# Performance work log

Hardware: AMD Instinct MI355X
Metric: run time of the kernel (lower is better)

## Reference

```python
import jax, jax.numpy as jnp
import numpy as np

DIM = 64
NUM_FEAT = 14
NUM_OUT = 105
N_NODES = 8192
N_EDGES = 16384
N_GRAPHS = 256
N_STEMS = 2048
N_JBONDS = 1024


def lrelu(v):
    return jax.nn.leaky_relu(v, 0.01)


def setup_inputs() -> dict:
    key = jax.random.key(0)
    ks = jax.random.split(key, 40)
    def rn(k, shape, s=0.1):
        return jax.random.normal(k, shape, dtype=jnp.float32) * s
    inp = {}
    inp['x'] = jax.random.normal(ks[0], (N_NODES, NUM_FEAT), dtype=jnp.float32)
    inp['edge_attr'] = jax.random.uniform(ks[1], (N_EDGES, 4), dtype=jnp.float32)
    inp['edge_index'] = jax.random.randint(ks[2], (2, N_EDGES), 0, N_NODES)
    inp['batch'] = jnp.sort(jax.random.randint(ks[3], (N_NODES,), 0, N_GRAPHS))
    inp['stem_atmidx'] = jax.random.randint(ks[4], (N_STEMS,), 0, N_NODES)
    inp['jbond_atmidx'] = jax.random.randint(ks[5], (N_JBONDS, 2), 0, N_NODES)
    # lin0
    inp['lin0_w'] = rn(ks[6], (NUM_FEAT, DIM)); inp['lin0_b'] = rn(ks[7], (DIM,))
    # NNConv edge net: Linear(4,dim) -> LeakyReLU -> Linear(dim, dim*dim)
    inp['net_w1'] = rn(ks[8], (4, DIM)); inp['net_b1'] = rn(ks[9], (DIM,))
    inp['net_w2'] = rn(ks[10], (DIM, DIM * DIM), 0.02); inp['net_b2'] = rn(ks[11], (DIM * DIM,), 0.02)
    # NNConv root weight + bias
    inp['conv_root'] = rn(ks[12], (DIM, DIM)); inp['conv_bias'] = rn(ks[13], (DIM,))
    # GRU (torch gate order r,z,n); stored [in, 3*dim]
    inp['gru_w_ih'] = rn(ks[14], (DIM, 3 * DIM)); inp['gru_w_hh'] = rn(ks[15], (DIM, 3 * DIM))
    inp['gru_b_ih'] = rn(ks[16], (3 * DIM,)); inp['gru_b_hh'] = rn(ks[17], (3 * DIM,))
    # node2stem MLP
    inp['n2s_w1'] = rn(ks[18], (DIM, DIM)); inp['n2s_b1'] = rn(ks[19], (DIM,))
    inp['n2s_w2'] = rn(ks[20], (DIM, NUM_OUT)); inp['n2s_b2'] = rn(ks[21], (NUM_OUT,))
    # node2jbond MLP
    inp['n2j_w1'] = rn(ks[22], (DIM, DIM)); inp['n2j_b1'] = rn(ks[23], (DIM,))
    inp['n2j_w2'] = rn(ks[24], (DIM, 1)); inp['n2j_b2'] = rn(ks[25], (1,))
    # Set2Set LSTM(2*dim -> dim), torch gate order i,f,g,o; stored [in, 4*dim]
    inp['s2s_w_ih'] = rn(ks[26], (2 * DIM, 4 * DIM)); inp['s2s_w_hh'] = rn(ks[27], (DIM, 4 * DIM))
    inp['s2s_b_ih'] = rn(ks[28], (4 * DIM,)); inp['s2s_b_hh'] = rn(ks[29], (4 * DIM,))
    # lin_out
    inp['lin_out_w'] = rn(ks[30], (2 * DIM, 2)); inp['lin_out_b'] = rn(ks[31], (2,))
    return inp


def reference(x, edge_attr, lin0_w, lin0_b, net_w1, net_b1, net_w2, net_b2,
              conv_root, conv_bias, gru_w_ih, gru_w_hh, gru_b_ih, gru_b_hh,
              n2s_w1, n2s_b1, n2s_w2, n2s_b2, n2j_w1, n2j_b1, n2j_w2, n2j_b2,
              s2s_w_ih, s2s_w_hh, s2s_b_ih, s2s_b_hh, lin_out_w, lin_out_b,
              edge_index, batch, stem_atmidx, jbond_atmidx):
    N = x.shape[0]
    src, dst = edge_index[0], edge_index[1]
    out = lrelu(x @ lin0_w + lin0_b)          # [N, dim]
    h = out
    # edge-conditioned weights (edge_attr is constant across the 6 iterations)
    ew = (lrelu(edge_attr @ net_w1 + net_b1) @ net_w2 + net_b2).reshape(-1, DIM, DIM)  # [E,dim,dim]
    deg = jnp.maximum(jax.ops.segment_sum(jnp.ones_like(dst, dtype=x.dtype), dst, num_segments=N), 1.0)[:, None]
    for _ in range(6):
        msg = jnp.einsum('ei,eio->eo', out[src], ew)                        # per-edge matmul
        agg = jax.ops.segment_sum(msg, dst, num_segments=N) / deg          # scatter-mean
        m = lrelu(agg + out @ conv_root + conv_bias)
        # GRU update (torch gate order r,z,n)
        gi = m @ gru_w_ih + gru_b_ih
        gh = h @ gru_w_hh + gru_b_hh
        ir, iz, inn = jnp.split(gi, 3, axis=-1)
        hr, hz, hn = jnp.split(gh, 3, axis=-1)
        r = jax.nn.sigmoid(ir + hr)
        z = jax.nn.sigmoid(iz + hz)
        n = jnp.tanh(inn + r * hn)
        h = (1.0 - z) * n + z * h
        out = h
    # per-stem block logits
    stem_preds = lrelu(out[stem_atmidx] @ n2s_w1 + n2s_b1) @ n2s_w2 + n2s_b2  # [S, num_out]
    # jbond: gather both endpoints, predict scalar, mean over the pair
    jb = out[jbond_atmidx.reshape(-1)]
    jpred = lrelu(jb @ n2j_w1 + n2j_b1) @ n2j_w2 + n2j_b2                     # [2J,1]
    jbond_preds = jpred.reshape(jbond_atmidx.shape).mean(axis=1)              # [J]
    # Set2Set, processing_steps=1
    B = N_GRAPHS
    hS = jnp.zeros((B, DIM), x.dtype)
    cS = jnp.zeros((B, DIM), x.dtype)
    q_star = jnp.zeros((B, 2 * DIM), x.dtype)
    gates = q_star @ s2s_w_ih + s2s_b_ih + hS @ s2s_w_hh + s2s_b_hh
    gi_, gf_, gg_, go_ = jnp.split(gates, 4, axis=-1)
    cS = jax.nn.sigmoid(gf_) * cS + jax.nn.sigmoid(gi_) * jnp.tanh(gg_)
    hS = jax.nn.sigmoid(go_) * jnp.tanh(cS)
    q = hS                                                                    # [B, dim]
    e = jnp.sum(out * q[batch], axis=-1)                                      # [N]
    emax = jax.ops.segment_max(e, batch, num_segments=B)
    a_un = jnp.exp(e - emax[batch])
    a = a_un / jax.ops.segment_sum(a_un, batch, num_segments=B)[batch]
    r_pool = jax.ops.segment_sum(a[:, None] * out, batch, num_segments=B)     # [B, dim]
    q_star = jnp.concatenate([q, r_pool], axis=1)                             # [B, 2*dim]
    scalar_outs = q_star @ lin_out_w + lin_out_b                              # [B, 2]
    return (scalar_outs, stem_preds, jbond_preds)
```

## Files before the change

### kernel.cpp

```cpp
#include <hip/hip_runtime.h>

#define DIM 64
#define NF 14
#define NOUT 105
#define NN 8192
#define NE 16384
#define NB 256
#define NS 2048
#define NJ 1024
#define KTOT 4160
#define KSPLIT 8

#define C_X      0
#define C_EA     114688
#define C_L0W    180224
#define C_L0B    181120
#define C_NW1    181184
#define C_NB1    181440
#define C_NW2    181504
#define C_NB2    443648
#define C_CRT    447744
#define C_CB     451840
#define C_GWIH   451904
#define C_GWHH   464192
#define C_GBIH   476480
#define C_GBHH   476672
#define C_SW1    476864
#define C_SB1    480960
#define C_SW2    481024
#define C_SB2    487744
#define C_JW1    487856
#define C_JB1    491952
#define C_JW2    492016
#define C_JB2    492080
#define C_S2IH   492088
#define C_S2HH   492344
#define C_LOW    492600
#define C_LOB    492856
#define C_TOT    492864

typedef float f32x4 __attribute__((ext_vector_type(4)));
typedef short bf16x8 __attribute__((ext_vector_type(8)));

__device__ __forceinline__ float bf2f(unsigned short u){
  union { unsigned int i; float f; } v; v.i = ((unsigned int)u) << 16; return v.f;
}
__device__ __forceinline__ unsigned short f2bf(float f){
  union { float f; unsigned int i; } v; v.f = f;
  unsigned int x = v.i;
  return (unsigned short)((x + 0x7FFFu + ((x >> 16) & 1u)) >> 16);
}
__device__ __forceinline__ float sigm(float x){ return 1.f / (1.f + __expf(-x)); }
__device__ __forceinline__ float tanh_f(float x){
  x = fminf(10.f, fmaxf(-10.f, x));
  float e = __expf(2.f * x);
  return (e - 1.f) / (e + 1.f);
}
__device__ __forceinline__ float lrelu(float x){ return x > 0.f ? x : 0.01f * x; }

__device__ __forceinline__ float wred_sum(float v){
  #pragma unroll
  for (int off = 32; off > 0; off >>= 1) v += __shfl_xor(v, off, 64);
  return v;
}
__device__ __forceinline__ float wred_max(float v){
  #pragma unroll
  for (int off = 32; off > 0; off >>= 1) v = fmaxf(v, __shfl_xor(v, off, 64));
  return v;
}


__global__ void k_detect(const unsigned short* __restrict__ ea, int* __restrict__ flag){
  __shared__ int cnt;
  if (threadIdx.x == 0) cnt = 0;
  __syncthreads();
  int c = 0;
  for (int i = threadIdx.x; i < 8192; i += 256) c += (ea[2*i] >> 15) & 1;
  atomicAdd(&cnt, c);
  __syncthreads();
  if (threadIdx.x == 0) *flag = (cnt > 100) ? 1 : 0;
}

struct CvtArgs {
  const void* src[26];
  int n[26];
  int off[26];
};

__global__ void k_cvt(CvtArgs a, const int* __restrict__ flag, unsigned short* __restrict__ dst){
  bool f32 = (*flag != 0);
  int gid = blockIdx.x * blockDim.x + threadIdx.x, gs = gridDim.x * blockDim.x;
  #pragma unroll 1
  for (int j = 0; j < 26; ++j){
    const void* s = a.src[j];
    int n = a.n[j], o = a.off[j];
    for (int i = gid; i < n; i += gs)
      dst[o + i] = f32 ? f2bf(((const float*)s)[i]) : ((const unsigned short*)s)[i];
  }
}

#define SETUP_BLOCKS 7249

__global__ __launch_bounds__(256) void k_setup(const unsigned short* __restrict__ cvt,
                       const int* __restrict__ ei, int big,
                       float* __restrict__ deg,
                       float* __restrict__ actF, unsigned short* __restrict__ actB,
                       unsigned short* __restrict__ z,
                       unsigned short* __restrict__ w2t, unsigned short* __restrict__ w2rt,
                       unsigned short* __restrict__ crt, unsigned short* __restrict__ btg,
                       float* __restrict__ cbg, float* __restrict__ qv){
  int bid = blockIdx.x, tid = threadIdx.x;
  if (bid < 2048){
    const unsigned short* x = cvt + C_X;
    const unsigned short* w = cvt + C_L0W;
    const unsigned short* b = cvt + C_L0B;
    int idx = bid * 256 + tid;
    int n = idx >> 6, d = idx & 63;
    float acc = bf2f(b[d]);
    #pragma unroll
    for (int f = 0; f < NF; ++f) acc += bf2f(x[n*NF + f]) * bf2f(w[f*DIM + d]);
    float v = lrelu(acc);
    actF[idx] = v; actB[idx] = f2bf(v);
  } else if (bid < 6144){
    const unsigned short* ea = cvt + C_EA;
    const unsigned short* w  = cvt + C_NW1;
    const unsigned short* b  = cvt + C_NB1;
    int idx = (bid - 2048) * 256 + tid;
    int e = idx >> 6, d = idx & 63;
    float acc = bf2f(b[d]);
    #pragma unroll
    for (int f = 0; f < 4; ++f) acc += bf2f(ea[e*4 + f]) * bf2f(w[f*DIM + d]);
    z[idx] = f2bf(lrelu(acc));
  } else if (bid < 7184){
    int idx = (bid - 6144) * 256 + tid;
    const unsigned short* w2 = cvt + C_NW2;
    if (big){
      if (idx < 4096*64){
        int n = idx >> 6, k = idx & 63;
        int c = ((n & 63) << 6) | (n >> 6);
        w2t[idx] = w2[k*4096 + c];
      }
    } else {
      if (idx < 64*KTOT){
        const unsigned short* b2 = cvt + C_NB2;
        int o = idx / KTOT, k = idx - o * KTOT;
        w2rt[idx] = (k < 4096) ? w2[(k >> 6) * 4096 + (k & 63) * 64 + o]
                               : b2[(k - 4096) * 64 + o];
      }
    }
  } else if (bid < 7248){
    int e = (bid - 7184) * 256 + tid;
    if (e < NE) atomicAdd(&deg[ei[NE + e]], 1.0f);
  } else {
    const unsigned short* cr  = cvt + C_CRT;
    const unsigned short* wih = cvt + C_GWIH;
    const unsigned short* whh = cvt + C_GWHH;
    const unsigned short* bih = cvt + C_GBIH;
    const unsigned short* bhh = cvt + C_GBHH;
    const unsigned short* s2sbih = cvt + C_S2IH;
    const unsigned short* s2sbhh = cvt + C_S2HH;
    for (int t = tid; t < 4096; t += 256){ int n = t & 63, k = t >> 6; crt[n*64 + k] = cr[k*64 + n]; }
    for (int t = tid; t < 32768; t += 256){
      int nidx = t >> 7, kidx = t & 127;
      int g = nidx >> 6, d = nidx & 63, ki = kidx & 63;
      unsigned short v = 0;
      if (kidx < 64){
        if (g == 0) v = wih[ki*192 + d];
        else if (g == 1) v = wih[ki*192 + 64 + d];
        else if (g == 2) v = wih[ki*192 + 128 + d];
      } else {
        if (g == 0) v = whh[ki*192 + d];
        else if (g == 1) v = whh[ki*192 + 64 + d];
        else if (g == 3) v = whh[ki*192 + 128 + d];
      }
      btg[nidx*128 + kidx] = v;
    }
    if (tid < 256){
      int g = tid >> 6, d = tid & 63;
      float v;
      if (g == 0) v = bf2f(bih[d]) + bf2f(bhh[d]);
      else if (g == 1) v = bf2f(bih[64 + d]) + bf2f(bhh[64 + d]);
      else if (g == 2) v = bf2f(bih[128 + d]);
      else v = bf2f(bhh[128 + d]);
      cbg[tid] = v;
    }
    if (tid < 64){
      float gi = bf2f(s2sbih[tid])       + bf2f(s2sbhh[tid]);
      float gg = bf2f(s2sbih[128 + tid]) + bf2f(s2sbhh[128 + tid]);
      float go = bf2f(s2sbih[192 + tid]) + bf2f(s2sbhh[192 + tid]);
      float c = sigm(gi) * tanh_f(gg);
      qv[tid] = sigm(go) * tanh_f(c);
    }
  }
}


__global__ __launch_bounds__(256) void k_ew(const unsigned short* __restrict__ z,
                                            const unsigned short* __restrict__ w2t,
                                            const unsigned short* __restrict__ cvt,
                                            unsigned short* __restrict__ ew){
  const unsigned short* b2 = cvt + C_NB2;
  int w = threadIdx.x >> 6, lane = threadIdx.x & 63;
  int lm = lane & 15, q8 = (lane >> 4) * 8, rq = (lane >> 4) * 4;
  int e0 = blockIdx.x * 64;
  int n0 = blockIdx.y * 256 + w * 64;
  f32x4 acc[4][4];
  #pragma unroll
  for (int mt = 0; mt < 4; ++mt)
    #pragma unroll
    for (int nt = 0; nt < 4; ++nt) acc[mt][nt] = (f32x4){0.f, 0.f, 0.f, 0.f};
  #pragma unroll
  for (int kk = 0; kk < 2; ++kk){
    bf16x8 af[4], bfr[4];
    #pragma unroll
    for (int mt = 0; mt < 4; ++mt)
      af[mt] = *(const bf16x8*)&z[(size_t)(e0 + mt*16 + lm)*64 + kk*32 + q8];
    #pragma unroll
    for (int nt = 0; nt < 4; ++nt)
      bfr[nt] = *(const bf16x8*)&w2t[(size_t)(n0 + nt*16 + lm)*64 + kk*32 + q8];
    #pragma unroll
    for (int mt = 0; mt < 4; ++mt)
      #pragma unroll
      for (int nt = 0; nt < 4; ++nt)
        acc[mt][nt] = __builtin_amdgcn_mfma_f32_16x16x32_bf16(af[mt], bfr[nt], acc[mt][nt], 0, 0, 0);
  }
  float bb[4]; int cols[4];
  #pragma unroll
  for (int nt = 0; nt < 4; ++nt){
    int dp = n0 + nt*16 + lm;
    cols[nt] = dp;
    bb[nt] = bf2f(b2[((dp & 63) << 6) | (dp >> 6)]);
  }
  #pragma unroll
  for (int mt = 0; mt < 4; ++mt)
    #pragma unroll
    for (int r = 0; r < 4; ++r){
      size_t rowb = (size_t)(e0 + mt*16 + rq + r) * 4096;
      #pragma unroll
      for (int nt = 0; nt < 4; ++nt)
        ew[rowb + cols[nt]] = f2bf(acc[mt][nt][r] + bb[nt]);
    }
}

__global__ __launch_bounds__(256) void k_msg(const float* __restrict__ actF,
                                             const unsigned short* __restrict__ ew,
                                             const int* __restrict__ ei,
                                             float* __restrict__ agg){
  int w = threadIdx.x >> 6, lane = threadIdx.x & 63;
  int e = blockIdx.x * 4 + w;
  int src = ei[e], dst = ei[NE + e];
  int g = lane >> 3;
  int s8 = (lane & 7) * 8;
  f32x4 a0 = *(const f32x4*)&actF[(size_t)src*64 + s8];
  f32x4 a1 = *(const f32x4*)&actF[(size_t)src*64 + s8 + 4];
  const unsigned short* ep = ew + (size_t)e * 4096;
  float po[8];
  #pragma unroll
  for (int j = 0; j < 8; ++j){
    bf16x8 v = *(const bf16x8*)&ep[(size_t)(j*8 + g)*64 + s8];
    const unsigned int* dw = (const unsigned int*)&v;
    float acc = 0.f;
    #pragma unroll
    for (int h = 0; h < 4; ++h){
      float flo = __uint_as_float(dw[h] << 16);
      float fhi = __uint_as_float(dw[h] & 0xFFFF0000u);
      float alo = (h < 2) ? a0[2*h]     : a1[2*h - 4];
      float ahi = (h < 2) ? a0[2*h + 1] : a1[2*h - 3];
      acc += flo * alo + fhi * ahi;
    }
    po[j] = acc;
  }
  #pragma unroll
  for (int j = 0; j < 8; ++j){
    po[j] += __shfl_xor(po[j], 1, 64);
    po[j] += __shfl_xor(po[j], 2, 64);
    po[j] += __shfl_xor(po[j], 4, 64);
  }
  if ((lane & 7) == 0){
    #pragma unroll
    for (int j = 0; j < 8; ++j)
      atomicAdd(&agg[(size_t)dst*64 + j*8 + g], po[j]);
  }
}


__global__ __launch_bounds__(256) void k_msgf(const unsigned short* __restrict__ actB,
                                              const unsigned short* __restrict__ z,
                                              const unsigned short* __restrict__ w2rt,
                                              const int* __restrict__ ei,
                                              float* __restrict__ agg){
  __shared__ __align__(16) unsigned short sz[256 * 8];
  int w = threadIdx.x >> 6, lane = threadIdx.x & 63;
  int lm = lane & 15, q8 = (lane >> 4) * 8, rq = (lane >> 4) * 4;
  int e0 = blockIdx.x * 256;
  int s  = blockIdx.y;
  {
    int t = threadIdx.x;
    *(uint4*)&sz[t * 8] = *(const uint4*)&z[(size_t)(e0 + t) * 64 + s * 8];
  }
  __syncthreads();

  uint4 apack[4][2];
  #pragma unroll
  for (int mt = 0; mt < 4; ++mt){
    int src = ei[e0 + w*64 + mt*16 + lm];
    apack[mt][0] = *(const uint4*)&actB[(size_t)src * 64 + q8];
    apack[mt][1] = *(const uint4*)&actB[(size_t)src * 64 + 32 + q8];
  }

  f32x4 acc[4][4];
  #pragma unroll
  for (int mt = 0; mt < 4; ++mt)
    #pragma unroll
    for (int nt = 0; nt < 4; ++nt) acc[mt][nt] = (f32x4){0.f, 0.f, 0.f, 0.f};

  int kk0 = s * 16;
  int nk = (s == KSPLIT - 1) ? 18 : 16;
  for (int c = 0; c < nk; ++c){
    int kk = kk0 + c;
    bf16x8 bfr[4];
    #pragma unroll
    for (int nt = 0; nt < 4; ++nt)
      bfr[nt] = *(const bf16x8*)&w2rt[(size_t)(nt*16 + lm) * KTOT + kk*32 + q8];
    #pragma unroll
    for (int mt = 0; mt < 4; ++mt){
      float zf = 1.0f;
      if (kk < 128){
        int erow = w*64 + mt*16 + lm;
        zf = bf2f(sz[erow * 8 + ((kk >> 1) & 7)]);
      }
      uint4 ap = apack[mt][kk & 1];
      bf16x8 af;
      #pragma unroll
      for (int h = 0; h < 4; ++h){
        unsigned int dw = ((const unsigned int*)&ap)[h];
        float flo = __uint_as_float(dw << 16) * zf;
        float fhi = __uint_as_float(dw & 0xFFFF0000u) * zf;
        unsigned int pk = ((unsigned int)f2bf(flo)) | (((unsigned int)f2bf(fhi)) << 16);
        ((unsigned int*)&af)[h] = pk;
      }
      #pragma unroll
      for (int nt = 0; nt < 4; ++nt)
        acc[mt][nt] = __builtin_amdgcn_mfma_f32_16x16x32_bf16(af, bfr[nt], acc[mt][nt], 0, 0, 0);
    }
  }

  #pragma unroll
  for (int mt = 0; mt < 4; ++mt){
    int dstv[4];
    #pragma unroll
    for (int r = 0; r < 4; ++r) dstv[r] = ei[NE + e0 + w*64 + mt*16 + rq + r];
    #pragma unroll
    for (int nt = 0; nt < 4; ++nt)
      #pragma unroll
      for (int r = 0; r < 4; ++r)
        atomicAdd(&agg[(size_t)dstv[r] * 64 + nt*16 + lm], acc[mt][nt][r]);
  }
}


__global__ __launch_bounds__(256) void k_gru(const unsigned short* __restrict__ actB_in,
                                             const float* __restrict__ actF_in,
                                             float* __restrict__ agg, const float* __restrict__ deg,
                                             const unsigned short* __restrict__ crt,
                                             const unsigned short* __restrict__ cvt,
                                             const unsigned short* __restrict__ btg,
                                             const float* __restrict__ cbg,
                                             float* __restrict__ actF_out, unsigned short* __restrict__ actB_out){
  const unsigned short* cbias = cvt + C_CB;
  __shared__ __align__(16) unsigned short s_frag[2*4*16*8];
  int w = threadIdx.x >> 6, lane = threadIdx.x & 63;
  int lm = lane & 15, q = lane >> 4;
  int q8 = q*8, rq = q*4;
  int r0 = blockIdx.x * 16;
  f32x4 am = (f32x4){0.f, 0.f, 0.f, 0.f};
  #pragma unroll
  for (int kk = 0; kk < 2; ++kk){
    bf16x8 a = *(const bf16x8*)&actB_in[(size_t)(r0 + lm)*64 + kk*32 + q8];
    bf16x8 b = *(const bf16x8*)&crt[(size_t)(w*16 + lm)*64 + kk*32 + q8];
    am = __builtin_amdgcn_mfma_f32_16x16x32_bf16(a, b, am, 0, 0, 0);
  }
  {
    int col = w*16 + lm;
    float cb = bf2f(cbias[col]);
    int kk2 = w >> 1, q2 = (w & 1)*2 + (lm >> 3), j = lm & 7;
    #pragma unroll
    for (int r = 0; r < 4; ++r){
      int row = r0 + rq + r;
      float dg = fmaxf(deg[row], 1.f);
      float v = am[r] + agg[(size_t)row*64 + col] / dg + cb;
      agg[(size_t)row*64 + col] = 0.f;
      s_frag[((kk2*4 + q2)*16 + (rq + r))*8 + j] = f2bf(lrelu(v));
    }
  }
  __syncthreads();
  f32x4 g[4];
  #pragma unroll
  for (int t = 0; t < 4; ++t) g[t] = (f32x4){0.f, 0.f, 0.f, 0.f};
  #pragma unroll
  for (int kk = 0; kk < 4; ++kk){
    bf16x8 a;
    if (kk < 2) a = *(const bf16x8*)&s_frag[(kk*4 + q)*128 + lm*8];
    else        a = *(const bf16x8*)&actB_in[(size_t)(r0 + lm)*64 + (kk - 2)*32 + q8];
    #pragma unroll
    for (int t = 0; t < 4; ++t){
      bf16x8 b = *(const bf16x8*)&btg[(size_t)(t*64 + w*16 + lm)*128 + kk*32 + q8];
      g[t] = __builtin_amdgcn_mfma_f32_16x16x32_bf16(a, b, g[t], 0, 0, 0);
    }
  }
  {
    int d = w*16 + lm;
    float cb_r = cbg[d], cb_z = cbg[64 + d], cb_n = cbg[128 + d], cb_h = cbg[192 + d];
    #pragma unroll
    for (int r = 0; r < 4; ++r){
      int row = r0 + rq + r;
      float rr = sigm(g[0][r] + cb_r);
      float zz = sigm(g[1][r] + cb_z);
      float nn = tanh_f(g[2][r] + cb_n + rr * (g[3][r] + cb_h));
      float ho = actF_in[(size_t)row*64 + d];
      float hn2 = (1.f - zz) * nn + zz * ho;
      actF_out[(size_t)row*64 + d] = hn2;
      actB_out[(size_t)row*64 + d] = f2bf(hn2);
    }
  }
}


__device__ __forceinline__ int lower_bound_batch(const int* b, int val){
  int lo = 0, hi = NN;
  while (lo < hi){ int mid = (lo + hi) >> 1; if (b[mid] < val) lo = mid + 1; else hi = mid; }
  return lo;
}

__device__ __forceinline__ void store_out(void* outp, const int* flag, size_t idx, float v){
  if (*flag) ((float*)outp)[idx] = v;
  else       ((unsigned short*)outp)[idx] = f2bf(v);
}

__global__ __launch_bounds__(256) void k_heads(const float* __restrict__ act,
                                               const int* __restrict__ batch,
                                               const float* __restrict__ qv,
                                               const int* __restrict__ sidx,
                                               const int* __restrict__ jidx,
                                               const unsigned short* __restrict__ cvt,
                                               const int* __restrict__ flag,
                                               void* __restrict__ outp){
  int bid = blockIdx.x;
  int w = threadIdx.x >> 6, lane = threadIdx.x & 63;
  if (bid < 512){
    const unsigned short* w1 = cvt + C_SW1;
    const unsigned short* b1 = cvt + C_SB1;
    const unsigned short* w2 = cvt + C_SW2;
    const unsigned short* b2 = cvt + C_SB2;
    __shared__ float sa[4][64], st[4][64];
    int s = bid * 4 + w;
    int a = sidx[s];
    sa[w][lane] = act[(size_t)a*64 + lane];
    __syncthreads();
    float t = bf2f(b1[lane]);
    #pragma unroll 8
    for (int i = 0; i < 64; ++i) t += sa[w][i] * bf2f(w1[i*64 + lane]);
    st[w][lane] = lrelu(t);
    __syncthreads();
    size_t base = 512 + (size_t)s * NOUT;
    float v = bf2f(b2[lane]);
    #pragma unroll 8
    for (int d = 0; d < 64; ++d) v += st[w][d] * bf2f(w2[d*NOUT + lane]);
    store_out(outp, flag, base + lane, v);
    int o2 = 64 + lane;
    if (o2 < NOUT){
      float v2 = bf2f(b2[o2]);
      #pragma unroll 8
      for (int d = 0; d < 64; ++d) v2 += st[w][d] * bf2f(w2[d*NOUT + o2]);
      store_out(outp, flag, base + o2, v2);
    }
  } else if (bid < 768){
    const unsigned short* w1 = cvt + C_JW1;
    const unsigned short* b1 = cvt + C_JB1;
    const unsigned short* w2 = cvt + C_JW2;
    const unsigned short* b2 = cvt + C_JB2;
    __shared__ float a0[4][64], a1[4][64];
    int j = (bid - 512) * 4 + w;
    int i0 = jidx[j*2], i1 = jidx[j*2 + 1];
    a0[w][lane] = act[(size_t)i0*64 + lane];
    a1[w][lane] = act[(size_t)i1*64 + lane];
    __syncthreads();
    float t0 = bf2f(b1[lane]), t1 = t0;
    #pragma unroll 8
    for (int i = 0; i < 64; ++i){
      float wv = bf2f(w1[i*64 + lane]);
      t0 += a0[w][i] * wv;
      t1 += a1[w][i] * wv;
    }
    t0 = lrelu(t0); t1 = lrelu(t1);
    float p = (t0 + t1) * bf2f(w2[lane]);
    p = wred_sum(p);
    if (lane == 0) store_out(outp, flag, 512 + (size_t)NS*NOUT + j, 0.5f * p + bf2f(b2[0]));
  } else {
    const unsigned short* lw = cvt + C_LOW;
    const unsigned short* lb = cvt + C_LOB;
    __shared__ float se[4][512];
    int b = (bid - 768) * 4 + w;
    int lo = lower_bound_batch(batch, b);
    int hi = lower_bound_batch(batch, b + 1);
    int cnt = hi - lo; if (cnt > 512) cnt = 512;
    float qvl = qv[lane];
    for (int ii = 0; ii < cnt; ++ii){
      float p = act[(size_t)(lo + ii)*64 + lane] * qvl;
      p = wred_sum(p);
      if (lane == 0) se[w][ii] = p;
    }
    __syncthreads();
    float em = -3.4e38f;
    for (int ii = lane; ii < cnt; ii += 64) em = fmaxf(em, se[w][ii]);
    em = wred_max(em);
    float sm = 0.f;
    for (int ii = lane; ii < cnt; ii += 64) sm += __expf(se[w][ii] - em);
    float denom = wred_sum(sm);
    float rp = 0.f;
    for (int ii = 0; ii < cnt; ++ii) rp += __expf(se[w][ii] - em) * act[(size_t)(lo + ii)*64 + lane];
    if (cnt > 0 && denom > 0.f) rp /= denom;
    float s0 = qvl*bf2f(lw[lane*2])     + rp*bf2f(lw[(64 + lane)*2]);
    float s1 = qvl*bf2f(lw[lane*2 + 1]) + rp*bf2f(lw[(64 + lane)*2 + 1]);
    s0 = wred_sum(s0); s1 = wred_sum(s1);
    if (lane == 0){
      store_out(outp, flag, b*2,     s0 + bf2f(lb[0]));
      store_out(outp, flag, b*2 + 1, s1 + bf2f(lb[1]));
    }
  }
}


extern "C" void kernel_launch(void* const* d_in, const int* in_sizes, int n_in,
                              void* d_out, int out_size, void* d_ws, size_t ws_size,
                              hipStream_t stream){
  (void)in_sizes; (void)n_in; (void)out_size;
  const int* edge_index = (const int*)d_in[2];
  const int* batch      = (const int*)d_in[3];
  const int* stem_idx   = (const int*)d_in[4];
  const int* jbond_idx  = (const int*)d_in[5];

  char* ws = (char*)d_ws;
  size_t off = 0;
  auto alloc = [&](size_t bytes) -> void* {
    void* p = ws + off; off += (bytes + 255) & ~(size_t)255; return p;
  };
  unsigned short* cvt  = (unsigned short*)alloc((size_t)C_TOT * 2);
  unsigned short* w2t  = (unsigned short*)alloc((size_t)4096 * 64 * 2);
  unsigned short* w2rt = (unsigned short*)alloc((size_t)64 * KTOT * 2);
  unsigned short* z_bf = (unsigned short*)alloc((size_t)NE * 64 * 2);
  float* actF0 = (float*)alloc((size_t)NN * 64 * 4);
  float* actF1 = (float*)alloc((size_t)NN * 64 * 4);
  unsigned short* actB0 = (unsigned short*)alloc((size_t)NN * 64 * 2);
  unsigned short* actB1 = (unsigned short*)alloc((size_t)NN * 64 * 2);
  float* deg  = (float*)alloc(NN * 4);
  float* agg  = (float*)alloc((size_t)NN * 64 * 4);
  unsigned short* crt = (unsigned short*)alloc(64 * 64 * 2);
  unsigned short* btg = (unsigned short*)alloc(256 * 128 * 2);
  float* cbg  = (float*)alloc(256 * 4);
  float* qv   = (float*)alloc(64 * 4);
  int* flag   = (int*)alloc(256);
  size_t ew_bytes = (size_t)NE * 4096 * 2;
  bool big = (off + ew_bytes) <= ws_size;
  unsigned short* ew = big ? (unsigned short*)alloc(ew_bytes) : nullptr;

  hipMemsetAsync(deg, 0, ((size_t)NN * 4) + ((size_t)NN * 64 * 4) + 256, stream);

  k_detect<<<1, 256, 0, stream>>>((const unsigned short*)d_in[1], flag);

  CvtArgs ca;
  const int srcIdx[26] = {0,1,6,7,8,9,10,11,12,13,14,15,16,17,18,19,20,21,22,23,24,25,28,29,30,31};
  const int ns[26]  = {114688,65536,896,64,256,64,262144,4096,4096,64,12288,12288,192,192,
                       4096,64,6720,105,4096,64,64,1,256,256,256,2};
  const int ofs[26] = {C_X,C_EA,C_L0W,C_L0B,C_NW1,C_NB1,C_NW2,C_NB2,C_CRT,C_CB,C_GWIH,C_GWHH,
                       C_GBIH,C_GBHH,C_SW1,C_SB1,C_SW2,C_SB2,C_JW1,C_JB1,C_JW2,C_JB2,
                       C_S2IH,C_S2HH,C_LOW,C_LOB};
  for (int j = 0; j < 26; ++j){ ca.src[j] = d_in[srcIdx[j]]; ca.n[j] = ns[j]; ca.off[j] = ofs[j]; }
  k_cvt<<<512, 256, 0, stream>>>(ca, flag, cvt);

  k_setup<<<SETUP_BLOCKS, 256, 0, stream>>>(cvt, edge_index, big ? 1 : 0, deg,
                                            actF0, actB0, z_bf, w2t, w2rt,
                                            crt, btg, cbg, qv);

  if (big)
    k_ew<<<dim3(NE/64, 16), 256, 0, stream>>>(z_bf, w2t, cvt, ew);

  for (int t = 0; t < 6; ++t){
    const float* aF_in  = (t & 1) ? actF1 : actF0;
    float* aF_out       = (t & 1) ? actF0 : actF1;
    const unsigned short* aB_in = (t & 1) ? actB1 : actB0;
    unsigned short* aB_out      = (t & 1) ? actB0 : actB1;
    if (big)
      k_msg<<<NE/4, 256, 0, stream>>>(aF_in, ew, edge_index, agg);
    else
      k_msgf<<<dim3(NE/256, KSPLIT), 256, 0, stream>>>(aB_in, z_bf, w2rt, edge_index, agg);
    k_gru<<<NN/16, 256, 0, stream>>>(aB_in, aF_in, agg, deg, crt, cvt, btg, cbg,
                                     aF_out, aB_out);
  }
  k_heads<<<832, 256, 0, stream>>>(actF0, batch, qv, stem_idx, jbond_idx, cvt, flag, d_out);
}
```

Before: 444.5 us.

## Replace atomic scatter aggregation with CSR-sorted messages and gather-reduce in GRU

Adds a single-block kernel that builds a CSR ordering of edges by destination and permutes z rows into sorted order, so the per-edge weight matrices are produced in destination order. The message kernel now writes per-edge messages without atomics, and the GRU kernel sums each node's contiguous messages, taking degree from the row pointers. This removes float atomic contention and the agg memset and deg pass. In exchange it adds a serial single-block CSR build and an extra message buffer round trip each step, and the k_msg inner loop now reads rows with a 128-byte lane stride.

```diff
diff --git a/kernel.cpp b/kernel.cpp
--- a/kernel.cpp
+++ b/kernel.cpp
@@ -99,11 +99,50 @@
   }
 }
 
-#define SETUP_BLOCKS 7249
+
+__global__ __launch_bounds__(1024) void k_csr(const int* __restrict__ ei,
+                                              int* __restrict__ rowptr, int* __restrict__ pos,
+                                              int* __restrict__ srcS, int* __restrict__ dstS){
+  __shared__ int cnt[NN];
+  __shared__ int part[1024];
+  int t = threadIdx.x;
+  for (int i = t; i < NN; i += 1024) cnt[i] = 0;
+  __syncthreads();
+  for (int e = t; e < NE; e += 1024) atomicAdd(&cnt[ei[NE + e]], 1);
+  __syncthreads();
+  int base = t * 8;
+  int loc[8];
+  int s = 0;
+  #pragma unroll
+  for (int k = 0; k < 8; ++k){ loc[k] = cnt[base + k]; s += loc[k]; }
+  part[t] = s;
+  __syncthreads();
+  for (int off = 1; off < 1024; off <<= 1){
+    int v = (t >= off) ? part[t - off] : 0;
+    __syncthreads();
+    part[t] += v;
+    __syncthreads();
+  }
+  int run = part[t] - s;
+  #pragma unroll
+  for (int k = 0; k < 8; ++k){ cnt[base + k] = run; run += loc[k]; }
+  __syncthreads();
+  for (int i = t; i < NN; i += 1024) rowptr[i] = cnt[i];
+  if (t == 0) rowptr[NN] = NE;
+  __syncthreads();
+  for (int e = t; e < NE; e += 1024){
+    int d = ei[NE + e];
+    int p = atomicAdd(&cnt[d], 1);
+    pos[e] = p;
+    srcS[p] = ei[e];
+    dstS[p] = d;
+  }
+}
+
+#define SETUP_BLOCKS 7185
 
 __global__ __launch_bounds__(256) void k_setup(const unsigned short* __restrict__ cvt,
-                       const int* __restrict__ ei, int big,
-                       float* __restrict__ deg,
+                       const int* __restrict__ pos, int big,
                        float* __restrict__ actF, unsigned short* __restrict__ actB,
                        unsigned short* __restrict__ z,
                        unsigned short* __restrict__ w2t, unsigned short* __restrict__ w2rt,
@@ -130,7 +169,7 @@
     float acc = bf2f(b[d]);
     #pragma unroll
     for (int f = 0; f < 4; ++f) acc += bf2f(ea[e*4 + f]) * bf2f(w[f*DIM + d]);
-    z[idx] = f2bf(lrelu(acc));
+    z[(size_t)pos[e]*64 + d] = f2bf(lrelu(acc));
   } else if (bid < 7184){
     int idx = (bid - 6144) * 256 + tid;
     const unsigned short* w2 = cvt + C_NW2;
@@ -148,9 +187,6 @@
                                : b2[(k - 4096) * 64 + o];
       }
     }
-  } else if (bid < 7248){
-    int e = (bid - 7184) * 256 + tid;
-    if (e < NE) atomicAdd(&deg[ei[NE + e]], 1.0f);
   } else {
     const unsigned short* cr  = cvt + C_CRT;
     const unsigned short* wih = cvt + C_GWIH;
@@ -244,50 +280,42 @@
 
 __global__ __launch_bounds__(256) void k_msg(const float* __restrict__ actF,
                                              const unsigned short* __restrict__ ew,
-                                             const int* __restrict__ ei,
-                                             float* __restrict__ agg){
+                                             const int* __restrict__ srcS,
+                                             float* __restrict__ msg){
+  __shared__ __align__(16) float sact[4][64];
   int w = threadIdx.x >> 6, lane = threadIdx.x & 63;
-  int e = blockIdx.x * 4 + w;
-  int src = ei[e], dst = ei[NE + e];
-  int g = lane >> 3;
-  int s8 = (lane & 7) * 8;
-  f32x4 a0 = *(const f32x4*)&actF[(size_t)src*64 + s8];
-  f32x4 a1 = *(const f32x4*)&actF[(size_t)src*64 + s8 + 4];
-  const unsigned short* ep = ew + (size_t)e * 4096;
-  float po[8];
+  int bid = blockIdx.x;
+  int swz = (bid & 7) * (NE/4/8) + (bid >> 3);
+  int slot = swz * 4 + w;
+  int src = srcS[slot];
+  sact[w][lane] = actF[(size_t)src*64 + lane];
+  __syncthreads();
+  const unsigned short* ep = ew + (size_t)slot * 4096;
+  float acc = 0.f;
   #pragma unroll
   for (int j = 0; j < 8; ++j){
-    bf16x8 v = *(const bf16x8*)&ep[(size_t)(j*8 + g)*64 + s8];
+    bf16x8 v = *(const bf16x8*)&ep[(size_t)lane*64 + j*8];
+    f32x4 alo = *(const f32x4*)&sact[w][j*8];
+    f32x4 ahi = *(const f32x4*)&sact[w][j*8 + 4];
     const unsigned int* dw = (const unsigned int*)&v;
-    float acc = 0.f;
-    #pragma unroll
-    for (int h = 0; h < 4; ++h){
-      float flo = __uint_as_float(dw[h] << 16);
-      float fhi = __uint_as_float(dw[h] & 0xFFFF0000u);
-      float alo = (h < 2) ? a0[2*h]     : a1[2*h - 4];
-      float ahi = (h < 2) ? a0[2*h + 1] : a1[2*h - 3];
-      acc += flo * alo + fhi * ahi;
-    }
-    po[j] = acc;
-  }
-  #pragma unroll
-  for (int j = 0; j < 8; ++j){
-    po[j] += __shfl_xor(po[j], 1, 64);
-    po[j] += __shfl_xor(po[j], 2, 64);
-    po[j] += __shfl_xor(po[j], 4, 64);
-  }
-  if ((lane & 7) == 0){
-    #pragma unroll
-    for (int j = 0; j < 8; ++j)
-      atomicAdd(&agg[(size_t)dst*64 + j*8 + g], po[j]);
-  }
+    acc += __uint_as_float(dw[0] << 16)          * alo[0];
+    acc += __uint_as_float(dw[0] & 0xFFFF0000u)  * alo[1];
+    acc += __uint_as_float(dw[1] << 16)          * alo[2];
+    acc += __uint_as_float(dw[1] & 0xFFFF0000u)  * alo[3];
+    acc += __uint_as_float(dw[2] << 16)          * ahi[0];
+    acc += __uint_as_float(dw[2] & 0xFFFF0000u)  * ahi[1];
+    acc += __uint_as_float(dw[3] << 16)          * ahi[2];
+    acc += __uint_as_float(dw[3] & 0xFFFF0000u)  * ahi[3];
+  }
+  msg[(size_t)slot*64 + lane] = acc;
 }
 
 
 __global__ __launch_bounds__(256) void k_msgf(const unsigned short* __restrict__ actB,
                                               const unsigned short* __restrict__ z,
                                               const unsigned short* __restrict__ w2rt,
-                                              const int* __restrict__ ei,
+                                              const int* __restrict__ srcS,
+                                              const int* __restrict__ dstS,
                                               float* __restrict__ agg){
   __shared__ __align__(16) unsigned short sz[256 * 8];
   int w = threadIdx.x >> 6, lane = threadIdx.x & 63;
@@ -303,7 +331,7 @@
   uint4 apack[4][2];
   #pragma unroll
   for (int mt = 0; mt < 4; ++mt){
-    int src = ei[e0 + w*64 + mt*16 + lm];
+    int src = srcS[e0 + w*64 + mt*16 + lm];
     apack[mt][0] = *(const uint4*)&actB[(size_t)src * 64 + q8];
     apack[mt][1] = *(const uint4*)&actB[(size_t)src * 64 + 32 + q8];
   }
@@ -349,7 +377,7 @@
   for (int mt = 0; mt < 4; ++mt){
     int dstv[4];
     #pragma unroll
-    for (int r = 0; r < 4; ++r) dstv[r] = ei[NE + e0 + w*64 + mt*16 + rq + r];
+    for (int r = 0; r < 4; ++r) dstv[r] = dstS[e0 + w*64 + mt*16 + rq + r];
     #pragma unroll
     for (int nt = 0; nt < 4; ++nt)
       #pragma unroll
@@ -361,7 +389,9 @@
 
 __global__ __launch_bounds__(256) void k_gru(const unsigned short* __restrict__ actB_in,
                                              const float* __restrict__ actF_in,
-                                             float* __restrict__ agg, const float* __restrict__ deg,
+                                             const float* __restrict__ msg,
+                                             const int* __restrict__ rowptr,
+                                             float* __restrict__ agg, int bigf,
                                              const unsigned short* __restrict__ crt,
                                              const unsigned short* __restrict__ cvt,
                                              const unsigned short* __restrict__ btg,
@@ -369,10 +399,30 @@
                                              float* __restrict__ actF_out, unsigned short* __restrict__ actB_out){
   const unsigned short* cbias = cvt + C_CB;
   __shared__ __align__(16) unsigned short s_frag[2*4*16*8];
+  __shared__ float aggT[16][65];
+  __shared__ int rp[17];
   int w = threadIdx.x >> 6, lane = threadIdx.x & 63;
   int lm = lane & 15, q = lane >> 4;
   int q8 = q*8, rq = q*4;
   int r0 = blockIdx.x * 16;
+  if (threadIdx.x < 17) rp[threadIdx.x] = rowptr[r0 + threadIdx.x];
+  __syncthreads();
+  if (bigf){
+    #pragma unroll
+    for (int k = 0; k < 4; ++k){
+      int ln = w*4 + k;
+      float acc = 0.f;
+      for (int s = rp[ln]; s < rp[ln+1]; ++s) acc += msg[(size_t)s*64 + lane];
+      aggT[ln][lane] = acc;
+    }
+  } else {
+    for (int idx = threadIdx.x; idx < 1024; idx += 256){
+      int ln = idx >> 6, c = idx & 63;
+      aggT[ln][c] = agg[(size_t)(r0+ln)*64 + c];
+      agg[(size_t)(r0+ln)*64 + c] = 0.f;
+    }
+  }
+  __syncthreads();
   f32x4 am = (f32x4){0.f, 0.f, 0.f, 0.f};
   #pragma unroll
   for (int kk = 0; kk < 2; ++kk){
@@ -386,11 +436,10 @@
     int kk2 = w >> 1, q2 = (w & 1)*2 + (lm >> 3), j = lm & 7;
     #pragma unroll
     for (int r = 0; r < 4; ++r){
-      int row = r0 + rq + r;
-      float dg = fmaxf(deg[row], 1.f);
-      float v = am[r] + agg[(size_t)row*64 + col] / dg + cb;
-      agg[(size_t)row*64 + col] = 0.f;
-      s_frag[((kk2*4 + q2)*16 + (rq + r))*8 + j] = f2bf(lrelu(v));
+      int lrow = rq + r;
+      float dg = fmaxf((float)(rp[lrow+1] - rp[lrow]), 1.f);
+      float v = am[r] + aggT[lrow][col] / dg + cb;
+      s_frag[((kk2*4 + q2)*16 + lrow)*8 + j] = f2bf(lrelu(v));
     }
   }
   __syncthreads();
@@ -553,8 +602,13 @@
   float* actF1 = (float*)alloc((size_t)NN * 64 * 4);
   unsigned short* actB0 = (unsigned short*)alloc((size_t)NN * 64 * 2);
   unsigned short* actB1 = (unsigned short*)alloc((size_t)NN * 64 * 2);
-  float* deg  = (float*)alloc(NN * 4);
-  float* agg  = (float*)alloc((size_t)NN * 64 * 4);
+  int* rowptr = (int*)alloc((size_t)(NN + 1) * 4);
+  int* pos    = (int*)alloc((size_t)NE * 4);
+  int* srcS   = (int*)alloc((size_t)NE * 4);
+  int* dstS   = (int*)alloc((size_t)NE * 4);
+  float* pool = (float*)alloc((size_t)NE * 64 * 4);
+  float* msg  = pool;
+  float* agg  = pool;
   unsigned short* crt = (unsigned short*)alloc(64 * 64 * 2);
   unsigned short* btg = (unsigned short*)alloc(256 * 128 * 2);
   float* cbg  = (float*)alloc(256 * 4);
@@ -564,7 +618,7 @@
   bool big = (off + ew_bytes) <= ws_size;
   unsigned short* ew = big ? (unsigned short*)alloc(ew_bytes) : nullptr;
 
-  hipMemsetAsync(deg, 0, ((size_t)NN * 4) + ((size_t)NN * 64 * 4) + 256, stream);
+  if (!big) hipMemsetAsync(agg, 0, (size_t)NN * 64 * 4, stream);
 
   k_detect<<<1, 256, 0, stream>>>((const unsigned short*)d_in[1], flag);
 
@@ -578,7 +632,9 @@
   for (int j = 0; j < 26; ++j){ ca.src[j] = d_in[srcIdx[j]]; ca.n[j] = ns[j]; ca.off[j] = ofs[j]; }
   k_cvt<<<512, 256, 0, stream>>>(ca, flag, cvt);
 
-  k_setup<<<SETUP_BLOCKS, 256, 0, stream>>>(cvt, edge_index, big ? 1 : 0, deg,
+  k_csr<<<1, 1024, 0, stream>>>(edge_index, rowptr, pos, srcS, dstS);
+
+  k_setup<<<SETUP_BLOCKS, 256, 0, stream>>>(cvt, pos, big ? 1 : 0,
                                             actF0, actB0, z_bf, w2t, w2rt,
                                             crt, btg, cbg, qv);
 
@@ -591,11 +647,11 @@
     const unsigned short* aB_in = (t & 1) ? actB1 : actB0;
     unsigned short* aB_out      = (t & 1) ? actB0 : actB1;
     if (big)
-      k_msg<<<NE/4, 256, 0, stream>>>(aF_in, ew, edge_index, agg);
+      k_msg<<<NE/4, 256, 0, stream>>>(aF_in, ew, srcS, msg);
     else
-      k_msgf<<<dim3(NE/256, KSPLIT), 256, 0, stream>>>(aB_in, z_bf, w2rt, edge_index, agg);
-    k_gru<<<NN/16, 256, 0, stream>>>(aB_in, aF_in, agg, deg, crt, cvt, btg, cbg,
-                                     aF_out, aB_out);
+      k_msgf<<<dim3(NE/256, KSPLIT), 256, 0, stream>>>(aB_in, z_bf, w2rt, srcS, dstS, agg);
+    k_gru<<<NN/16, 256, 0, stream>>>(aB_in, aF_in, msg, rowptr, agg, big ? 1 : 0,
+                                     crt, cvt, btg, cbg, aF_out, aB_out);
   }
   k_heads<<<832, 256, 0, stream>>>(actF0, batch, qv, stem_idx, jbond_idx, cvt, flag, d_out);
 }
```

Measured after the change: 519.5 us. +16.9%, slower.

## Replace materialized per-edge weight tensor with fused on-the-fly NNConv message GEMM

Applied to the files above, without the earlier changes.

Removes the path that precomputes a 16384x4096 bf16 per-edge weight tensor (about 128 MB, written once and then read in each of the six message passes). Message computation now always goes through a fused kernel that forms the outer product of edge features and source activations and multiplies it by the reordered second-layer weights with MFMA. That kernel stages weight chunks in LDS with register prefetch, uses 64 edges per block with no K-split, and packs values with a hardware bf16 convert instruction. The change trades a large amount of memory traffic for more MFMA work per pass, plus two block barriers per chunk.

```diff
diff --git a/kernel.cpp b/kernel.cpp
--- a/kernel.cpp
+++ b/kernel.cpp
@@ -9,7 +9,6 @@
 #define NS 2048
 #define NJ 1024
 #define KTOT 4160
-#define KSPLIT 8
 
 #define C_X      0
 #define C_EA     114688
@@ -102,11 +101,11 @@
 #define SETUP_BLOCKS 7249
 
 __global__ __launch_bounds__(256) void k_setup(const unsigned short* __restrict__ cvt,
-                       const int* __restrict__ ei, int big,
+                       const int* __restrict__ ei,
                        float* __restrict__ deg,
                        float* __restrict__ actF, unsigned short* __restrict__ actB,
                        unsigned short* __restrict__ z,
-                       unsigned short* __restrict__ w2t, unsigned short* __restrict__ w2rt,
+                       unsigned short* __restrict__ w2rt,
                        unsigned short* __restrict__ crt, unsigned short* __restrict__ btg,
                        float* __restrict__ cbg, float* __restrict__ qv){
   int bid = blockIdx.x, tid = threadIdx.x;
@@ -134,20 +133,10 @@
   } else if (bid < 7184){
     int idx = (bid - 6144) * 256 + tid;
     const unsigned short* w2 = cvt + C_NW2;
-    if (big){
-      if (idx < 4096*64){
-        int n = idx >> 6, k = idx & 63;
-        int c = ((n & 63) << 6) | (n >> 6);
-        w2t[idx] = w2[k*4096 + c];
-      }
-    } else {
-      if (idx < 64*KTOT){
-        const unsigned short* b2 = cvt + C_NB2;
-        int o = idx / KTOT, k = idx - o * KTOT;
-        w2rt[idx] = (k < 4096) ? w2[(k >> 6) * 4096 + (k & 63) * 64 + o]
-                               : b2[(k - 4096) * 64 + o];
-      }
-    }
+    const unsigned short* b2 = cvt + C_NB2;
+    int o = idx / KTOT, k = idx - o * KTOT;
+    w2rt[idx] = (k < 4096) ? w2[(k >> 6) * 4096 + (k & 63) * 64 + o]
+                           : b2[(k - 4096) * 64 + o];
   } else if (bid < 7248){
     int e = (bid - 7184) * 256 + tid;
     if (e < NE) atomicAdd(&deg[ei[NE + e]], 1.0f);
@@ -195,167 +184,104 @@
 }
 
 
-__global__ __launch_bounds__(256) void k_ew(const unsigned short* __restrict__ z,
-                                            const unsigned short* __restrict__ w2t,
-                                            const unsigned short* __restrict__ cvt,
-                                            unsigned short* __restrict__ ew){
-  const unsigned short* b2 = cvt + C_NB2;
-  int w = threadIdx.x >> 6, lane = threadIdx.x & 63;
+__global__ __launch_bounds__(256) void k_msg(const unsigned short* __restrict__ actB,
+                                             const unsigned short* __restrict__ z,
+                                             const unsigned short* __restrict__ w2rt,
+                                             const int* __restrict__ ei,
+                                             float* __restrict__ agg){
+  __shared__ __align__(16) unsigned short sB[64*264];
+  __shared__ __align__(16) unsigned short sz[64*72];
+  int tid = threadIdx.x;
+  int w = tid >> 6, lane = tid & 63;
   int lm = lane & 15, q8 = (lane >> 4) * 8, rq = (lane >> 4) * 4;
   int e0 = blockIdx.x * 64;
-  int n0 = blockIdx.y * 256 + w * 64;
-  f32x4 acc[4][4];
-  #pragma unroll
-  for (int mt = 0; mt < 4; ++mt)
-    #pragma unroll
-    for (int nt = 0; nt < 4; ++nt) acc[mt][nt] = (f32x4){0.f, 0.f, 0.f, 0.f};
-  #pragma unroll
-  for (int kk = 0; kk < 2; ++kk){
-    bf16x8 af[4], bfr[4];
-    #pragma unroll
-    for (int mt = 0; mt < 4; ++mt)
-      af[mt] = *(const bf16x8*)&z[(size_t)(e0 + mt*16 + lm)*64 + kk*32 + q8];
-    #pragma unroll
-    for (int nt = 0; nt < 4; ++nt)
-      bfr[nt] = *(const bf16x8*)&w2t[(size_t)(n0 + nt*16 + lm)*64 + kk*32 + q8];
-    #pragma unroll
-    for (int mt = 0; mt < 4; ++mt)
+  {
+    int edge = tid >> 2, quarter = tid & 3;
+    const uint4* s = (const uint4*)&z[(size_t)(e0 + edge)*64 + quarter*16];
+    uint4* d = (uint4*)&sz[edge*72 + quarter*16];
+    d[0] = s[0]; d[1] = s[1];
+  }
+  int erow = w*16 + lm;
+  int srcn = ei[e0 + erow];
+  uint4 apack0 = *(const uint4*)&actB[(size_t)srcn*64 + q8];
+  uint4 apack1 = *(const uint4*)&actB[(size_t)srcn*64 + 32 + q8];
+
+  uint4 pf[8];
+  #pragma unroll
+  for (int u = 0; u < 8; ++u){
+    int v = tid + u*256;
+    pf[u] = *(const uint4*)&w2rt[(size_t)(v >> 5)*KTOT + (v & 31)*8];
+  }
+  f32x4 acc[4];
+  #pragma unroll
+  for (int nt = 0; nt < 4; ++nt) acc[nt] = (f32x4){0.f, 0.f, 0.f, 0.f};
+
+  #pragma unroll 1
+  for (int c = 0; c < 16; ++c){
+    __syncthreads();
+    #pragma unroll
+    for (int u = 0; u < 8; ++u){
+      int v = tid + u*256;
+      *(uint4*)&sB[(v >> 5)*264 + (v & 31)*8] = pf[u];
+    }
+    __syncthreads();
+    if (c < 15){
+      int c0k = (c + 1) * 256;
       #pragma unroll
-      for (int nt = 0; nt < 4; ++nt)
-        acc[mt][nt] = __builtin_amdgcn_mfma_f32_16x16x32_bf16(af[mt], bfr[nt], acc[mt][nt], 0, 0, 0);
-  }
-  float bb[4]; int cols[4];
-  #pragma unroll
-  for (int nt = 0; nt < 4; ++nt){
-    int dp = n0 + nt*16 + lm;
-    cols[nt] = dp;
-    bb[nt] = bf2f(b2[((dp & 63) << 6) | (dp >> 6)]);
-  }
-  #pragma unroll
-  for (int mt = 0; mt < 4; ++mt)
-    #pragma unroll
-    for (int r = 0; r < 4; ++r){
-      size_t rowb = (size_t)(e0 + mt*16 + rq + r) * 4096;
+      for (int u = 0; u < 8; ++u){
+        int v = tid + u*256;
+        pf[u] = *(const uint4*)&w2rt[(size_t)(v >> 5)*KTOT + c0k + (v & 31)*8];
+      }
+    }
+    #pragma unroll
+    for (int kk2L = 0; kk2L < 4; ++kk2L){
+      float zf = bf2f(sz[erow*72 + c*4 + kk2L]);
       #pragma unroll
-      for (int nt = 0; nt < 4; ++nt)
-        ew[rowb + cols[nt]] = f2bf(acc[mt][nt][r] + bb[nt]);
-    }
-}
-
-__global__ __launch_bounds__(256) void k_msg(const float* __restrict__ actF,
-                                             const unsigned short* __restrict__ ew,
-                                             const int* __restrict__ ei,
-                                             float* __restrict__ agg){
-  int w = threadIdx.x >> 6, lane = threadIdx.x & 63;
-  int e = blockIdx.x * 4 + w;
-  int src = ei[e], dst = ei[NE + e];
-  int g = lane >> 3;
-  int s8 = (lane & 7) * 8;
-  f32x4 a0 = *(const f32x4*)&actF[(size_t)src*64 + s8];
-  f32x4 a1 = *(const f32x4*)&actF[(size_t)src*64 + s8 + 4];
-  const unsigned short* ep = ew + (size_t)e * 4096;
-  float po[8];
-  #pragma unroll
-  for (int j = 0; j < 8; ++j){
-    bf16x8 v = *(const bf16x8*)&ep[(size_t)(j*8 + g)*64 + s8];
-    const unsigned int* dw = (const unsigned int*)&v;
-    float acc = 0.f;
-    #pragma unroll
-    for (int h = 0; h < 4; ++h){
-      float flo = __uint_as_float(dw[h] << 16);
-      float fhi = __uint_as_float(dw[h] & 0xFFFF0000u);
-      float alo = (h < 2) ? a0[2*h]     : a1[2*h - 4];
-      float ahi = (h < 2) ? a0[2*h + 1] : a1[2*h - 3];
-      acc += flo * alo + fhi * ahi;
-    }
-    po[j] = acc;
-  }
-  #pragma unroll
-  for (int j = 0; j < 8; ++j){
-    po[j] += __shfl_xor(po[j], 1, 64);
-    po[j] += __shfl_xor(po[j], 2, 64);
-    po[j] += __shfl_xor(po[j], 4, 64);
-  }
-  if ((lane & 7) == 0){
-    #pragma unroll
-    for (int j = 0; j < 8; ++j)
-      atomicAdd(&agg[(size_t)dst*64 + j*8 + g], po[j]);
-  }
-}
-
-
-__global__ __launch_bounds__(256) void k_msgf(const unsigned short* __restrict__ actB,
-                                              const unsigned short* __restrict__ z,
-                                              const unsigned short* __restrict__ w2rt,
-                                              const int* __restrict__ ei,
-                                              float* __restrict__ agg){
-  __shared__ __align__(16) unsigned short sz[256 * 8];
-  int w = threadIdx.x >> 6, lane = threadIdx.x & 63;
-  int lm = lane & 15, q8 = (lane >> 4) * 8, rq = (lane >> 4) * 4;
-  int e0 = blockIdx.x * 256;
-  int s  = blockIdx.y;
-  {
-    int t = threadIdx.x;
-    *(uint4*)&sz[t * 8] = *(const uint4*)&z[(size_t)(e0 + t) * 64 + s * 8];
+      for (int half = 0; half < 2; ++half){
+        const unsigned int* ap = (const unsigned int*)(half ? &apack1 : &apack0);
+        bf16x8 af;
+        #pragma unroll
+        for (int h = 0; h < 4; ++h){
+          float flo = __uint_as_float(ap[h] << 16) * zf;
+          float fhi = __uint_as_float(ap[h] & 0xFFFF0000u) * zf;
+          unsigned int pk;
+          asm("v_cvt_pk_bf16_f32 %0, %1, %2" : "=v"(pk) : "v"(flo), "v"(fhi));
+          ((unsigned int*)&af)[h] = pk;
+        }
+        int colb = (kk2L*2 + half)*32 + q8;
+        #pragma unroll
+        for (int nt = 0; nt < 4; ++nt){
+          bf16x8 bfr = *(const bf16x8*)&sB[(nt*16 + lm)*264 + colb];
+          acc[nt] = __builtin_amdgcn_mfma_f32_16x16x32_bf16(af, bfr, acc[nt], 0, 0, 0);
+        }
+      }
+    }
   }
   __syncthreads();
-
-  uint4 apack[4][2];
-  #pragma unroll
-  for (int mt = 0; mt < 4; ++mt){
-    int src = ei[e0 + w*64 + mt*16 + lm];
-    apack[mt][0] = *(const uint4*)&actB[(size_t)src * 64 + q8];
-    apack[mt][1] = *(const uint4*)&actB[(size_t)src * 64 + 32 + q8];
-  }
-
-  f32x4 acc[4][4];
-  #pragma unroll
-  for (int mt = 0; mt < 4; ++mt)
-    #pragma unroll
-    for (int nt = 0; nt < 4; ++nt) acc[mt][nt] = (f32x4){0.f, 0.f, 0.f, 0.f};
-
-  int kk0 = s * 16;
-  int nk = (s == KSPLIT - 1) ? 18 : 16;
-  for (int c = 0; c < nk; ++c){
-    int kk = kk0 + c;
-    bf16x8 bfr[4];
-    #pragma unroll
-    for (int nt = 0; nt < 4; ++nt)
-      bfr[nt] = *(const bf16x8*)&w2rt[(size_t)(nt*16 + lm) * KTOT + kk*32 + q8];
-    #pragma unroll
-    for (int mt = 0; mt < 4; ++mt){
-      float zf = 1.0f;
-      if (kk < 128){
-        int erow = w*64 + mt*16 + lm;
-        zf = bf2f(sz[erow * 8 + ((kk >> 1) & 7)]);
-      }
-      uint4 ap = apack[mt][kk & 1];
-      bf16x8 af;
-      #pragma unroll
-      for (int h = 0; h < 4; ++h){
-        unsigned int dw = ((const unsigned int*)&ap)[h];
-        float flo = __uint_as_float(dw << 16) * zf;
-        float fhi = __uint_as_float(dw & 0xFFFF0000u) * zf;
-        unsigned int pk = ((unsigned int)f2bf(flo)) | (((unsigned int)f2bf(fhi)) << 16);
-        ((unsigned int*)&af)[h] = pk;
-      }
-      #pragma unroll
-      for (int nt = 0; nt < 4; ++nt)
-        acc[mt][nt] = __builtin_amdgcn_mfma_f32_16x16x32_bf16(af, bfr[nt], acc[mt][nt], 0, 0, 0);
-    }
-  }
-
-  #pragma unroll
-  for (int mt = 0; mt < 4; ++mt){
-    int dstv[4];
-    #pragma unroll
-    for (int r = 0; r < 4; ++r) dstv[r] = ei[NE + e0 + w*64 + mt*16 + rq + r];
-    #pragma unroll
-    for (int nt = 0; nt < 4; ++nt)
-      #pragma unroll
-      for (int r = 0; r < 4; ++r)
-        atomicAdd(&agg[(size_t)dstv[r] * 64 + nt*16 + lm], acc[mt][nt][r]);
-  }
+  #pragma unroll
+  for (int u = 0; u < 2; ++u){
+    int v = tid + u*256;
+    *(uint4*)&sB[(v >> 3)*264 + (v & 7)*8] = *(const uint4*)&w2rt[(size_t)(v >> 3)*KTOT + 4096 + (v & 7)*8];
+  }
+  __syncthreads();
+  #pragma unroll
+  for (int half = 0; half < 2; ++half){
+    bf16x8 af = half ? *(const bf16x8*)&apack1 : *(const bf16x8*)&apack0;
+    int colb = half*32 + q8;
+    #pragma unroll
+    for (int nt = 0; nt < 4; ++nt){
+      bf16x8 bfr = *(const bf16x8*)&sB[(nt*16 + lm)*264 + colb];
+      acc[nt] = __builtin_amdgcn_mfma_f32_16x16x32_bf16(af, bfr, acc[nt], 0, 0, 0);
+    }
+  }
+  int dstv[4];
+  #pragma unroll
+  for (int r = 0; r < 4; ++r) dstv[r] = ei[NE + e0 + w*16 + rq + r];
+  #pragma unroll
+  for (int nt = 0; nt < 4; ++nt)
+    #pragma unroll
+    for (int r = 0; r < 4; ++r)
+      atomicAdd(&agg[(size_t)dstv[r]*64 + nt*16 + lm], acc[nt][r]);
 }
 
 
@@ -534,7 +460,7 @@
 extern "C" void kernel_launch(void* const* d_in, const int* in_sizes, int n_in,
                               void* d_out, int out_size, void* d_ws, size_t ws_size,
                               hipStream_t stream){
-  (void)in_sizes; (void)n_in; (void)out_size;
+  (void)in_sizes; (void)n_in; (void)out_size; (void)ws_size;
   const int* edge_index = (const int*)d_in[2];
   const int* batch      = (const int*)d_in[3];
   const int* stem_idx   = (const int*)d_in[4];
@@ -546,7 +472,6 @@
     void* p = ws + off; off += (bytes + 255) & ~(size_t)255; return p;
   };
   unsigned short* cvt  = (unsigned short*)alloc((size_t)C_TOT * 2);
-  unsigned short* w2t  = (unsigned short*)alloc((size_t)4096 * 64 * 2);
   unsigned short* w2rt = (unsigned short*)alloc((size_t)64 * KTOT * 2);
   unsigned short* z_bf = (unsigned short*)alloc((size_t)NE * 64 * 2);
   float* actF0 = (float*)alloc((size_t)NN * 64 * 4);
@@ -560,11 +485,8 @@
   float* cbg  = (float*)alloc(256 * 4);
   float* qv   = (float*)alloc(64 * 4);
   int* flag   = (int*)alloc(256);
-  size_t ew_bytes = (size_t)NE * 4096 * 2;
-  bool big = (off + ew_bytes) <= ws_size;
-  unsigned short* ew = big ? (unsigned short*)alloc(ew_bytes) : nullptr;
-
-  hipMemsetAsync(deg, 0, ((size_t)NN * 4) + ((size_t)NN * 64 * 4) + 256, stream);
+
+  hipMemsetAsync(deg, 0, ((size_t)NN * 4) + ((size_t)NN * 64 * 4), stream);
 
   k_detect<<<1, 256, 0, stream>>>((const unsigned short*)d_in[1], flag);
 
@@ -578,22 +500,16 @@
   for (int j = 0; j < 26; ++j){ ca.src[j] = d_in[srcIdx[j]]; ca.n[j] = ns[j]; ca.off[j] = ofs[j]; }
   k_cvt<<<512, 256, 0, stream>>>(ca, flag, cvt);
 
-  k_setup<<<SETUP_BLOCKS, 256, 0, stream>>>(cvt, edge_index, big ? 1 : 0, deg,
-                                            actF0, actB0, z_bf, w2t, w2rt,
+  k_setup<<<SETUP_BLOCKS, 256, 0, stream>>>(cvt, edge_index, deg,
+                                            actF0, actB0, z_bf, w2rt,
                                             crt, btg, cbg, qv);
-
-  if (big)
-    k_ew<<<dim3(NE/64, 16), 256, 0, stream>>>(z_bf, w2t, cvt, ew);
 
   for (int t = 0; t < 6; ++t){
     const float* aF_in  = (t & 1) ? actF1 : actF0;
     float* aF_out       = (t & 1) ? actF0 : actF1;
     const unsigned short* aB_in = (t & 1) ? actB1 : actB0;
     unsigned short* aB_out      = (t & 1) ? actB0 : actB1;
-    if (big)
-      k_msg<<<NE/4, 256, 0, stream>>>(aF_in, ew, edge_index, agg);
-    else
-      k_msgf<<<dim3(NE/256, KSPLIT), 256, 0, stream>>>(aB_in, z_bf, w2rt, edge_index, agg);
+    k_msg<<<NE/64, 256, 0, stream>>>(aB_in, z_bf, w2rt, edge_index, agg);
     k_gru<<<NN/16, 256, 0, stream>>>(aB_in, aF_in, agg, deg, crt, cvt, btg, cbg,
                                      aF_out, aB_out);
   }
```

Result: slower. 556.5 us (+25.2%).
